# Kernel optimization log

Hardware: AMD Instinct MI355X
Metric: run time of the kernel (lower is better)

Reference implementation:

```python
import jax, jax.numpy as jnp
import numpy as np

B, LP, LQ, H = 16, 1024, 1024, 1024


def setup_inputs() -> dict:
    key = jax.random.key(0)
    k1, k2, k3 = jax.random.split(key, 3)
    p = jax.random.normal(k1, (B, LP, H), dtype=jnp.float32)
    q = jax.random.normal(k2, (B, LQ, H), dtype=jnp.float32)
    # Dense(hidden_size) kernel + bias (glorot-ish scale)
    W_key = jax.random.normal(k3, (H, H), dtype=jnp.float32) / np.sqrt(H)
    b_key = jnp.zeros((H,), dtype=jnp.float32)
    return {"p": p, "q": q, "W_key": W_key, "b_key": b_key}


def reference(p, q, W_key, b_key):
    # keys = Dense(q): [B, LQ, H]
    keys = jnp.einsum("bqh,hk->bqk", q, W_key) + b_key
    # attention scores p @ keys^T (no scaling): [B, LP, LQ]
    scores = jnp.einsum("bph,bqh->bpq", p, keys)
    attn = jax.nn.softmax(scores, axis=-1)
    # q reused as values; relu on output: [B, LP, H]
    out = jax.nn.relu(jnp.einsum("bpq,bqh->bph", attn, q))
    return out
```

## Files before the change

kernel.cpp:

```cpp
#include <hip/hip_runtime.h>
#include <hip/hip_bf16.h>

#define B_N 16
#define LP_N 1024
#define LQ_N 1024
#define H_N 1024

typedef unsigned short u16;
typedef __attribute__((ext_vector_type(8))) _Float16 f16x8;
typedef __attribute__((ext_vector_type(4))) float f32x4;

__device__ __forceinline__ u16 f2h(float x) {
    _Float16 h = (_Float16)x;
    return *(u16*)&h;
}
__device__ __forceinline__ float h2f(u16 u) {
    _Float16 h;
    *(u16*)&h = u;
    return (float)h;
}

__device__ __forceinline__ void load_lds16(const u16* g, u16* l) {
    __builtin_amdgcn_global_load_lds(
        (const __attribute__((address_space(1))) void*)g,
        (__attribute__((address_space(3))) void*)l, 16, 0, 0);
}

#define MFMA_F16(a, b, c) __builtin_amdgcn_mfma_f32_16x16x32_f16(a, b, c, 0, 0, 0)
#define VMW0()  asm volatile("s_waitcnt vmcnt(0)" ::: "memory")
#define LGKM8() asm volatile("s_waitcnt lgkmcnt(8)" ::: "memory")
#define LGKM0() asm volatile("s_waitcnt lgkmcnt(0)" ::: "memory")
#define SCHB()  __builtin_amdgcn_sched_barrier(0)
#define SBAR()  __builtin_amdgcn_s_barrier()

template<bool SPLIT, int EPI>
__launch_bounds__(512, 2)
__global__ void gemm2t(const u16* __restrict__ Ahi, const u16* __restrict__ Alo,
                       const u16* __restrict__ Bm,
                       const float* __restrict__ bias,
                       float* __restrict__ Cf, u16* __restrict__ Ch,
                       int N, int gn, int gmn,
                       long long sA, long long sB, long long sC)
{
    constexpr int REG  = 8192;
    constexpr int O_AL = REG;
    constexpr int O_B  = SPLIT ? 2 * REG : REG;
    constexpr int BUF  = SPLIT ? 3 * REG : 2 * REG;
    __shared__ __align__(16) u16 lds[2 * BUF];

    const int tid  = threadIdx.x;
    const int lane = tid & 63;
    const int wv   = tid >> 6;
    const int wr   = wv >> 2, wc = wv & 3;

    const int d   = blockIdx.x;
    const int cpx = gridDim.x >> 3;
    const int swz = (d & 7) * cpx + (d >> 3);
    const long long z = swz / gmn;
    const int r_  = swz % gmn;
    const int bm  = (r_ / gn) * 256;
    const int bn  = (r_ % gn) * 256;

    const char* pAh = (const char*)(Ahi + z * sA);
    const char* pAl = (const char*)(Alo + z * sA);
    const char* pB  = (const char*)(Bm + z * sB);

    const int r0 = tid >> 2;
    const int xc = (tid & 3) ^ ((r0 >> 1) & 3);
    const long long aof = (long long)(bm + r0) * 2048 + xc * 16;
    const long long bof = (long long)(bn + r0) * 2048 + xc * 16;
    const long long ao2 = aof + 128 * 2048;
    const long long bo2 = bof + 128 * 2048;
    const int d0 = tid * 8;
    const int d1 = d0 + 4096;

    int offA[8], offB[4];
#pragma unroll
    for (int i = 0; i < 8; ++i) {
        const int r = wr * 128 + i * 16 + (lane & 15);
        offA[i] = r * 32 + ((((lane >> 4) ^ (r >> 1)) & 3) << 3);
    }
#pragma unroll
    for (int j = 0; j < 4; ++j) {
        const int r = wc * 64 + j * 16 + (lane & 15);
        offB[j] = r * 32 + ((((lane >> 4) ^ (r >> 1)) & 3) << 3);
    }

    f32x4 acc[8][4];
#pragma unroll
    for (int i = 0; i < 8; ++i)
#pragma unroll
        for (int j = 0; j < 4; ++j)
            acc[i][j] = (f32x4){0.f, 0.f, 0.f, 0.f};

#define STG(NB, KB) do {                                                      \
        load_lds16((const u16*)(pAh + aof + (KB)), lds + (NB) + d0);          \
        load_lds16((const u16*)(pAh + ao2 + (KB)), lds + (NB) + d1);          \
        load_lds16((const u16*)(pB + bof + (KB)), lds + (NB) + O_B + d0);     \
        load_lds16((const u16*)(pB + bo2 + (KB)), lds + (NB) + O_B + d1);     \
        if constexpr (SPLIT) {                                                \
            load_lds16((const u16*)(pAl + aof + (KB)), lds + (NB) + O_AL + d0); \
            load_lds16((const u16*)(pAl + ao2 + (KB)), lds + (NB) + O_AL + d1); \
        }                                                                     \
    } while (0)

#define TERM(AF, BF) do {                                                     \
        __builtin_amdgcn_s_setprio(1);                                        \
        _Pragma("unroll")                                                     \
        for (int i = 0; i < 8; ++i)                                           \
            _Pragma("unroll")                                                 \
            for (int j = 0; j < 4; ++j)                                       \
                acc[i][j] = MFMA_F16(AF[i], BF[j], acc[i][j]);                \
        __builtin_amdgcn_s_setprio(0);                                        \
    } while (0)

    constexpr int NT = 32;

    STG(0, 0);

    for (int t = 0; t < NT; ++t) {
        const int cb = (t & 1) ? BUF : 0;
        const int nb = (t & 1) ? 0 : BUF;
        const long long kb = (long long)(t + 1) * 64;

        VMW0();
        SBAR();
        f16x8 b[4], ah[8], al[8];
#pragma unroll
        for (int j = 0; j < 4; ++j)
            b[j] = *(const f16x8*)(lds + cb + O_B + offB[j]);
#pragma unroll
        for (int i = 0; i < 8; ++i)
            ah[i] = *(const f16x8*)(lds + cb + offA[i]);
        if constexpr (SPLIT) {
#pragma unroll
            for (int i = 0; i < 8; ++i)
                al[i] = *(const f16x8*)(lds + cb + O_AL + offA[i]);
        }
        if (t + 1 < NT) STG(nb, kb);
        if constexpr (SPLIT) { LGKM8(); } else { LGKM0(); }
        SCHB();
        TERM(ah, b);
        if constexpr (SPLIT) {
            LGKM0(); SCHB();
            TERM(al, b);
        }
    }
#undef STG
#undef TERM

    const long long Cbase = z * sC;
#pragma unroll
    for (int i = 0; i < 8; ++i) {
        const int row0 = bm + wr * 128 + i * 16 + ((lane >> 4) << 2);
#pragma unroll
        for (int j = 0; j < 4; ++j) {
            const int col = bn + wc * 64 + j * 16 + (lane & 15);
#pragma unroll
            for (int e = 0; e < 4; ++e) {
                const float v = acc[i][j][e];
                const long long idx = Cbase + (long long)(row0 + e) * N + col;
                if constexpr (EPI == 0) {
                    Cf[idx] = v;
                } else if constexpr (EPI == 1) {
                    Ch[idx] = f2h(v + bias[col]);
                } else {
                    Cf[idx] = fmaxf(v, 0.f);
                }
            }
        }
    }
}

__global__ void cvt_f16(const float* __restrict__ in, u16* __restrict__ o16,
                        long long n4)
{
    const long long i = (long long)blockIdx.x * 256 + threadIdx.x;
    if (i >= n4) return;
    const float4 v = ((const float4*)in)[i];
    ushort4 h;
    h.x = f2h(v.x); h.y = f2h(v.y); h.z = f2h(v.z); h.w = f2h(v.w);
    ((ushort4*)o16)[i] = h;
}

__global__ void fuse_cvt_q(const float* __restrict__ q, u16* __restrict__ hi,
                           u16* __restrict__ lo, u16* __restrict__ thi)
{
    __shared__ float t[32][33];
    const long long z = blockIdx.z;
    const long long base = z * 1048576;
    const int r0 = blockIdx.y * 32, c0 = blockIdx.x * 32;
    for (int j = threadIdx.y; j < 32; j += 8) {
        const float v = q[base + (long long)(r0 + j) * 1024 + c0 + threadIdx.x];
        t[j][threadIdx.x] = v;
        const long long o = base + (long long)(r0 + j) * 1024 + c0 + threadIdx.x;
        const u16 h = f2h(v);
        hi[o] = h;
        lo[o] = f2h(v - h2f(h));
    }
    __syncthreads();
    for (int j = threadIdx.y; j < 32; j += 8)
        thi[base + (long long)(c0 + j) * 1024 + r0 + threadIdx.x] = f2h(t[threadIdx.x][j]);
}

__global__ void transpose_cvt_w(const float* __restrict__ in, u16* __restrict__ hi)
{
    __shared__ float t[32][33];
    const int r0 = blockIdx.y * 32, c0 = blockIdx.x * 32;
    for (int j = threadIdx.y; j < 32; j += 8)
        t[j][threadIdx.x] = in[(long long)(r0 + j) * 1024 + c0 + threadIdx.x];
    __syncthreads();
    for (int j = threadIdx.y; j < 32; j += 8)
        hi[(long long)(c0 + j) * 1024 + r0 + threadIdx.x] = f2h(t[threadIdx.x][j]);
}

__global__ void softmax_f16(const float* __restrict__ S, u16* __restrict__ A)
{
    const long long row = blockIdx.x;
    const float* r = S + row * (long long)LQ_N;
    const int t = threadIdx.x;
    float4 v = ((const float4*)r)[t];

    float m = fmaxf(fmaxf(v.x, v.y), fmaxf(v.z, v.w));
#pragma unroll
    for (int off = 32; off > 0; off >>= 1)
        m = fmaxf(m, __shfl_xor(m, off));

    __shared__ float red[4];
    const int lane = t & 63, wid = t >> 6;
    if (lane == 0) red[wid] = m;
    __syncthreads();
    m = fmaxf(fmaxf(red[0], red[1]), fmaxf(red[2], red[3]));
    __syncthreads();

    v.x = __expf(v.x - m); v.y = __expf(v.y - m);
    v.z = __expf(v.z - m); v.w = __expf(v.w - m);
    float s = v.x + v.y + v.z + v.w;
#pragma unroll
    for (int off = 32; off > 0; off >>= 1)
        s += __shfl_xor(s, off);
    if (lane == 0) red[wid] = s;
    __syncthreads();
    s = red[0] + red[1] + red[2] + red[3];

    const float inv = 1.0f / s;
    ushort4 o;
    o.x = f2h(v.x * inv); o.y = f2h(v.y * inv);
    o.z = f2h(v.z * inv); o.w = f2h(v.w * inv);
    ((ushort4*)(A + row * (long long)LQ_N))[t] = o;
}

#define BM 128
#define BN 128
#define BK 8
#define TM 8
#define TN 8

template<bool TRANSB, bool BIAS, bool RELU>
__launch_bounds__(256)
__global__ void gemm_k(const float* __restrict__ A, const float* __restrict__ Bmat,
                       const float* __restrict__ bias, float* __restrict__ C,
                       int M, int N, int K,
                       long long sA, long long sB, long long sC)
{
    __shared__ float As[BK][BM];
    __shared__ float Bs[BK][BN];
    const int tid = threadIdx.x;
    const int tx = tid & 15;
    const int ty = tid >> 4;
    const int bn = blockIdx.x * BN;
    const int bm = blockIdx.y * BM;
    const long long z = blockIdx.z;
    A += z * sA; Bmat += z * sB; C += z * sC;
    float acc[TM][TN];
#pragma unroll
    for (int i = 0; i < TM; i++)
#pragma unroll
        for (int j = 0; j < TN; j++) acc[i][j] = 0.f;
    const int arow = tid >> 1;
    const int acol = (tid & 1) * 4;
    const int bk_n = tid >> 5;
    const int bn_n = (tid & 31) * 4;
    for (int k0 = 0; k0 < K; k0 += BK) {
        float4 a4 = *(const float4*)&A[(long long)(bm + arow) * K + k0 + acol];
        As[acol + 0][arow] = a4.x; As[acol + 1][arow] = a4.y;
        As[acol + 2][arow] = a4.z; As[acol + 3][arow] = a4.w;
        if (TRANSB) {
            float4 b4 = *(const float4*)&Bmat[(long long)(bn + arow) * K + k0 + acol];
            Bs[acol + 0][arow] = b4.x; Bs[acol + 1][arow] = b4.y;
            Bs[acol + 2][arow] = b4.z; Bs[acol + 3][arow] = b4.w;
        } else {
            float4 b4 = *(const float4*)&Bmat[(long long)(k0 + bk_n) * N + bn + bn_n];
            *(float4*)&Bs[bk_n][bn_n] = b4;
        }
        __syncthreads();
#pragma unroll
        for (int k = 0; k < BK; k++) {
            float a[TM], b[TN];
            *(float4*)&a[0] = *(const float4*)&As[k][ty * TM];
            *(float4*)&a[4] = *(const float4*)&As[k][ty * TM + 4];
            *(float4*)&b[0] = *(const float4*)&Bs[k][tx * TN];
            *(float4*)&b[4] = *(const float4*)&Bs[k][tx * TN + 4];
#pragma unroll
            for (int i = 0; i < TM; i++)
#pragma unroll
                for (int j = 0; j < TN; j++)
                    acc[i][j] = fmaf(a[i], b[j], acc[i][j]);
        }
        __syncthreads();
    }
#pragma unroll
    for (int i = 0; i < TM; i++) {
        const int row = bm + ty * TM + i;
#pragma unroll
        for (int j = 0; j < TN; j += 4) {
            const int col = bn + tx * TN + j;
            float4 v;
            v.x = acc[i][j + 0]; v.y = acc[i][j + 1];
            v.z = acc[i][j + 2]; v.w = acc[i][j + 3];
            if (BIAS) {
                v.x += bias[col + 0]; v.y += bias[col + 1];
                v.z += bias[col + 2]; v.w += bias[col + 3];
            }
            if (RELU) {
                v.x = fmaxf(v.x, 0.f); v.y = fmaxf(v.y, 0.f);
                v.z = fmaxf(v.z, 0.f); v.w = fmaxf(v.w, 0.f);
            }
            *(float4*)&C[(long long)row * N + col] = v;
        }
    }
}

__global__ void softmax_k(float* __restrict__ S)
{
    const long long row = blockIdx.x;
    float* r = S + row * (long long)LQ_N;
    const int t = threadIdx.x;
    float4 v = ((float4*)r)[t];
    float m = fmaxf(fmaxf(v.x, v.y), fmaxf(v.z, v.w));
#pragma unroll
    for (int off = 32; off > 0; off >>= 1)
        m = fmaxf(m, __shfl_xor(m, off));
    __shared__ float red[4];
    const int lane = t & 63, wid = t >> 6;
    if (lane == 0) red[wid] = m;
    __syncthreads();
    m = fmaxf(fmaxf(red[0], red[1]), fmaxf(red[2], red[3]));
    __syncthreads();
    v.x = __expf(v.x - m); v.y = __expf(v.y - m);
    v.z = __expf(v.z - m); v.w = __expf(v.w - m);
    float s = v.x + v.y + v.z + v.w;
#pragma unroll
    for (int off = 32; off > 0; off >>= 1)
        s += __shfl_xor(s, off);
    if (lane == 0) red[wid] = s;
    __syncthreads();
    s = red[0] + red[1] + red[2] + red[3];
    const float inv = 1.0f / s;
    v.x *= inv; v.y *= inv; v.z *= inv; v.w *= inv;
    ((float4*)r)[t] = v;
}

extern "C" void kernel_launch(void* const* d_in, const int* in_sizes, int n_in,
                              void* d_out, int out_size, void* d_ws, size_t ws_size,
                              hipStream_t stream)
{
    const float* p    = (const float*)d_in[0];
    const float* q    = (const float*)d_in[1];
    const float* W    = (const float*)d_in[2];
    const float* bias = (const float*)d_in[3];
    float* out = (float*)d_out;

    const size_t MB32 = 33554432ull;
    const size_t NEED = 5 * MB32 + 2097152ull;

    if (ws_size >= NEED) {
        char* w = (char*)d_ws;
        u16* p16   = (u16*)(w + 0 * MB32);
        u16* q_hi  = (u16*)(w + 1 * MB32);
        u16* q_lo  = (u16*)(w + 2 * MB32);
        u16* keys  = (u16*)(w + 3 * MB32);
        u16* qT    = (u16*)(w + 4 * MB32);
        u16* Wt    = (u16*)(w + 5 * MB32);
        float* scores = (float*)(w + 1 * MB32);
        u16* attn     = (u16*)(w + 0 * MB32);

        const long long n4 = (long long)B_N * LQ_N * H_N / 4;
        cvt_f16<<<dim3((unsigned)(n4 / 256)), 256, 0, stream>>>(p, p16, n4);
        fuse_cvt_q<<<dim3(32, 32, B_N), dim3(32, 8), 0, stream>>>(q, q_hi, q_lo, qT);
        transpose_cvt_w<<<dim3(32, 32, 1), dim3(32, 8), 0, stream>>>(W, Wt);

        gemm2t<true, 1><<<256, 512, 0, stream>>>(
            q_hi, q_lo, Wt, bias, nullptr, keys,
            H_N, 4, 256, 0, 0, 0);

        gemm2t<false, 0><<<256, 512, 0, stream>>>(
            p16, p16, keys, nullptr, scores, nullptr,
            LQ_N, 4, 16,
            (long long)LP_N * H_N, (long long)LQ_N * H_N, (long long)LP_N * LQ_N);

        softmax_f16<<<B_N * LP_N, 256, 0, stream>>>(scores, attn);

        gemm2t<false, 2><<<256, 512, 0, stream>>>(
            attn, attn, qT, nullptr, out, nullptr,
            H_N, 4, 16,
            (long long)LP_N * LQ_N, (long long)H_N * LQ_N, (long long)LP_N * H_N);
    } else {
        float* keys   = (float*)d_ws;
        float* scores = keys + (long long)B_N * LQ_N * H_N;

        gemm_k<false, true, false><<<dim3(H_N / BN, (B_N * LQ_N) / BM, 1), 256, 0, stream>>>(
            q, W, bias, keys, B_N * LQ_N, H_N, H_N, 0, 0, 0);
        gemm_k<true, false, false><<<dim3(LQ_N / BN, LP_N / BM, B_N), 256, 0, stream>>>(
            p, keys, nullptr, scores, LP_N, LQ_N, H_N,
            (long long)LP_N * H_N, (long long)LQ_N * H_N, (long long)LP_N * LQ_N);
        softmax_k<<<B_N * LP_N, 256, 0, stream>>>(scores);
        gemm_k<false, false, true><<<dim3(H_N / BN, LP_N / BM, B_N), 256, 0, stream>>>(
            scores, q, nullptr, out, LP_N, H_N, LQ_N,
            (long long)LP_N * LQ_N, (long long)LQ_N * H_N, (long long)LP_N * H_N);
    }
}
```

Before: 231.5 us.

## Load A operand directly from global into registers in batched GEMMs

Result: slower. 310.2 us (+34.0%).

```diff
diff --git a/kernel.cpp b/kernel.cpp
--- a/kernel.cpp
+++ b/kernel.cpp
@@ -167,6 +167,141 @@
                 } else {
                     Cf[idx] = fmaxf(v, 0.f);
                 }
+            }
+        }
+    }
+}
+
+template<int EPI>
+__launch_bounds__(512, 1)
+__global__ void gemm_da(const u16* __restrict__ Am, const u16* __restrict__ Bm,
+                        float* __restrict__ Cf,
+                        int N, int gn, int gmn,
+                        long long sA, long long sB, long long sC)
+{
+    constexpr int BUF = 8192;
+    __shared__ __align__(16) u16 lds[2 * BUF];
+
+    const int tid  = threadIdx.x;
+    const int lane = tid & 63;
+    const int wv   = tid >> 6;
+    const int wr   = wv >> 2, wc = wv & 3;
+
+    const int d   = blockIdx.x;
+    const int cpx = gridDim.x >> 3;
+    const int swz = (d & 7) * cpx + (d >> 3);
+    const long long z = swz / gmn;
+    const int r_  = swz % gmn;
+    const int bm  = (r_ / gn) * 256;
+    const int bn  = (r_ % gn) * 256;
+
+    const char* pA = (const char*)(Am + z * sA);
+    const char* pB = (const char*)(Bm + z * sB);
+
+    const int r0 = tid >> 2;
+    const int xc = (tid & 3) ^ ((r0 >> 1) & 3);
+    const long long bof  = (long long)(bn + r0) * 2048 + xc * 16;
+    const long long bof2 = bof + 128 * 2048;
+    const int d0 = tid * 8;
+    const int d1 = d0 + 4096;
+
+    int offB[4];
+#pragma unroll
+    for (int j = 0; j < 4; ++j) {
+        const int r = wc * 64 + j * 16 + (lane & 15);
+        offB[j] = r * 32 + ((((lane >> 4) ^ (r >> 1)) & 3) << 3);
+    }
+
+    const long long aoff0 = (long long)(bm + wr * 128 + (lane & 15)) * 2048
+                          + ((lane >> 4) << 4);
+
+    f32x4 acc[8][4];
+#pragma unroll
+    for (int i = 0; i < 8; ++i)
+#pragma unroll
+        for (int j = 0; j < 4; ++j)
+            acc[i][j] = (f32x4){0.f, 0.f, 0.f, 0.f};
+
+    f16x8 aP[8], aQ[8];
+
+#define STGB(NB, KB) do {                                                     \
+        load_lds16((const u16*)(pB + bof  + (KB)), lds + (NB) + d0);          \
+        load_lds16((const u16*)(pB + bof2 + (KB)), lds + (NB) + d1);          \
+    } while (0)
+
+#define LOADA(DST, KB) do {                                                   \
+        _Pragma("unroll")                                                     \
+        for (int i = 0; i < 8; ++i)                                           \
+            DST[i] = *(const f16x8*)(pA + aoff0 + (long long)i * 32768 + (KB)); \
+    } while (0)
+
+#define RD_B(B_, CB) do {                                                     \
+        _Pragma("unroll")                                                     \
+        for (int j = 0; j < 4; ++j)                                           \
+            B_[j] = *(const f16x8*)(lds + (CB) + offB[j]);                    \
+    } while (0)
+
+#define TERM(AF, BF) do {                                                     \
+        __builtin_amdgcn_s_setprio(1);                                        \
+        _Pragma("unroll")                                                     \
+        for (int i = 0; i < 8; ++i)                                           \
+            _Pragma("unroll")                                                 \
+            for (int j = 0; j < 4; ++j)                                       \
+                acc[i][j] = MFMA_F16(AF[i], BF[j], acc[i][j]);                \
+        __builtin_amdgcn_s_setprio(0);                                        \
+    } while (0)
+
+    constexpr int NT = 32;
+
+    STGB(0, 0);
+    LOADA(aP, 0);
+
+    for (int t = 0; t < NT; t += 2) {
+        {
+            VMW0();
+            SBAR();
+            f16x8 b[4];
+            RD_B(b, 0);
+            if (t + 1 < NT) {
+                const long long kb = (long long)(t + 1) * 64;
+                STGB(BUF, kb);
+                LOADA(aQ, kb);
+            }
+            LGKM0(); SCHB();
+            TERM(aP, b);
+        }
+        {
+            VMW0();
+            SBAR();
+            f16x8 b[4];
+            RD_B(b, BUF);
+            if (t + 2 < NT) {
+                const long long kb = (long long)(t + 2) * 64;
+                STGB(0, kb);
+                LOADA(aP, kb);
+            }
+            LGKM0(); SCHB();
+            TERM(aQ, b);
+        }
+    }
+#undef STGB
+#undef LOADA
+#undef RD_B
+#undef TERM
+
+    const long long Cbase = z * sC;
+#pragma unroll
+    for (int i = 0; i < 8; ++i) {
+        const int row0 = bm + wr * 128 + i * 16 + ((lane >> 4) << 2);
+#pragma unroll
+        for (int j = 0; j < 4; ++j) {
+            const int col = bn + wc * 64 + j * 16 + (lane & 15);
+#pragma unroll
+            for (int e = 0; e < 4; ++e) {
+                const float v = acc[i][j][e];
+                const long long idx = Cbase + (long long)(row0 + e) * N + col;
+                if constexpr (EPI == 0) Cf[idx] = v;
+                else                    Cf[idx] = fmaxf(v, 0.f);
             }
         }
     }
@@ -394,15 +529,15 @@
             q_hi, q_lo, Wt, bias, nullptr, keys,
             H_N, 4, 256, 0, 0, 0);
 
-        gemm2t<false, 0><<<256, 512, 0, stream>>>(
-            p16, p16, keys, nullptr, scores, nullptr,
+        gemm_da<0><<<256, 512, 0, stream>>>(
+            p16, keys, scores,
             LQ_N, 4, 16,
             (long long)LP_N * H_N, (long long)LQ_N * H_N, (long long)LP_N * LQ_N);
 
         softmax_f16<<<B_N * LP_N, 256, 0, stream>>>(scores, attn);
 
-        gemm2t<false, 2><<<256, 512, 0, stream>>>(
-            attn, attn, qT, nullptr, out, nullptr,
+        gemm_da<2><<<256, 512, 0, stream>>>(
+            attn, qT, out,
             H_N, 4, 16,
             (long long)LP_N * LQ_N, (long long)H_N * LQ_N, (long long)LP_N * H_N);
     } else {
```
